# Kernel optimization log

Hardware: AMD Instinct MI355X
Metric: run time of the kernel (lower is better)

## Reference

```python
import jax, jax.numpy as jnp
import numpy as np

NUM_INPUTS = 784
NUM_OUTPUTS = 784
WIDTH_POW = 10
WIDTH = 2 ** WIDTH_POW          # 1024
HALF = WIDTH // 2               # 512
DEPTH = 8
BDEPTH = 10
DEGREE = 2
BATCH = 4096

# knots from the source: tensor([-256..256]) / 32
_KNOTS = np.array([-256., -128., -64., -32., -16., -8., -4., -2., -1., 0.,
                   1., 2., 4., 8., 16., 32., 64., 128., 256.], dtype=np.float32) / 32.0
# clamped (open) knot vector: repeat endpoints `degree` times
_T = np.concatenate([np.full(DEGREE, _KNOTS[0]), _KNOTS, np.full(DEGREE, _KNOTS[-1])]).astype(np.float32)
SPLINE_DIM = len(_T) - DEGREE - 1  # 20 basis functions


def _bspline_basis(x):
    """Cox-de Boor B-spline basis, vectorized over all elements of x.
    Returns basis of shape x.shape + (SPLINE_DIM,)."""
    t = jnp.asarray(_T)
    x = jnp.clip(x, _T[0], _T[-1] - 1e-6)  # clamp to knot span (eval domain)
    xe = x[..., None]
    B = ((xe >= t[:-1]) & (xe < t[1:])).astype(x.dtype)  # degree-0 indicators
    for k in range(1, DEGREE + 1):
        tj, tjk = t[:-(k + 1)], t[k:-1]
        tj1, tjk1 = t[1:-k], t[k + 1:]
        d1, d2 = tjk - tj, tjk1 - tj1
        w1 = jnp.where(d1 > 0, (xe - tj) / jnp.where(d1 > 0, d1, 1.0), 0.0)
        w2 = jnp.where(d2 > 0, (tjk1 - xe) / jnp.where(d2 > 0, d2, 1.0), 0.0)
        B = w1 * B[..., :-1] + w2 * B[..., 1:]
    return B  # [..., SPLINE_DIM]


def _butterfly(X, params):
    """OrthogonalButterfly.forward. params: [HALF, BDEPTH]. X: [B, WIDTH]."""
    Bsz = X.shape[0]
    for d in range(BDEPTH):
        theta = params[:, d]
        c, s = jnp.cos(theta), jnp.sin(theta)
        X0, X1 = X[:, :HALF], X[:, HALF:]
        n0 = X0 * c + X1 * s
        n1 = -X0 * s + X1 * c
        # perm[i] = i//2 (even) / i//2 + half (odd) == interleave halves
        X = jnp.stack([n0, n1], axis=2).reshape(Bsz, WIDTH)
    return X


def _forward(X, butterfly_params, spline_coefs):
    Bsz = X.shape[0]
    X = jnp.concatenate([X, jnp.zeros((Bsz, WIDTH - NUM_INPUTS), X.dtype)], axis=1)
    for i in range(DEPTH):
        X = _butterfly(X, butterfly_params[i])
        if i != DEPTH - 1:
            # ReversibleActivation: X0 += spline(X1), per-column spline coefs
            X0, X1 = X[:, :HALF], X[:, HALF:]
            act = jnp.einsum('bwd,wd->bw', _bspline_basis(X1), spline_coefs[i])
            X = jnp.concatenate([X0 + act, X1], axis=1)
    return X[:, :NUM_OUTPUTS]


def setup_inputs() -> dict:
    key = jax.random.key(0)
    k1, k2, k3 = jax.random.split(key, 3)
    X = jax.random.normal(k1, (BATCH, NUM_INPUTS), dtype=jnp.float32)
    butterfly_params = jax.random.uniform(k2, (DEPTH, HALF, BDEPTH), dtype=jnp.float32) * (2.0 * np.pi)
    spline_coefs = jax.random.uniform(k3, (DEPTH - 1, HALF, SPLINE_DIM), dtype=jnp.float32) * 0.2 - 0.1
    return {"X": X, "butterfly_params": butterfly_params, "spline_coefs": spline_coefs}


def reference(X, butterfly_params, spline_coefs):
    return _forward(X, butterfly_params, spline_coefs)
```

## Files before the change

### kernel.cpp

```cpp
#include <hip/hip_runtime.h>

#define NIN 784
#define WIDTH 1024
#define HALF 512
#define DEPTH 8
#define BDEPTH 10
#define BATCH 4096
#define SPLINE_DIM 20
#define NQ 18

__device__ float d_T[23] = {
  -8.f, -8.f, -8.f, -4.f, -2.f, -1.f, -0.5f, -0.25f, -0.125f, -0.0625f,
  -0.03125f, 0.f, 0.03125f, 0.0625f, 0.125f, 0.25f, 0.5f, 1.f, 2.f, 4.f,
  8.f, 8.f, 8.f };

__global__ void prep_kernel(const float* __restrict__ bp,
                            const float* __restrict__ sc,
                            float2* __restrict__ cs,
                            float4* __restrict__ qt) {
  int gid = blockIdx.x * 256 + threadIdx.x;
  if (gid < DEPTH * BDEPTH * 1024) {
    int slot = gid & 1023;
    int d = (gid >> 10) % BDEPTH;
    int i = gid / (BDEPTH * 1024);
    int n = 0;
#pragma unroll
    for (int b = 0; b < 10; ++b) {
      int src = b - d; if (src < 0) src += 10;
      n |= ((slot >> src) & 1) << b;
    }
    int pj = n & 511;
    float theta = bp[(i * HALF + pj) * BDEPTH + d];
    float c = cosf(theta), s = sinf(theta);
    cs[gid] = make_float2(c, (n & 512) ? -s : s);
  }
  int gid2 = gid - DEPTH * BDEPTH * 1024;
  if (gid2 >= 0 && gid2 < (DEPTH - 1) * NQ * HALF) {
    int w = gid2 & 511;
    int mi = (gid2 >> 9) % NQ;
    int i = gid2 / (NQ * HALF);
    int m = mi + 2;
    const float* cf = sc + (i * HALF + w) * SPLINE_DIM;
    double c0 = cf[mi], c1 = cf[mi + 1], c2 = cf[mi + 2];
    double tm1 = d_T[m - 1], tm = d_T[m], tp1 = d_T[m + 1], tp2 = d_T[m + 2];
    double h = tp1 - tm;
    double us[3] = { 0.0, 0.5 * h, 0.75 * h };
    double y[3];
#pragma unroll
    for (int k = 0; k < 3; ++k) {
      double x = tm + us[k];
      double left1 = x - tm, right1 = tp1 - x, left2 = x - tm1, right2 = tp2 - x;
      double inv1 = 1.0 / (tp1 - tm);
      double N0 = right1 * inv1, N1 = left1 * inv1;
      double temp0 = N0 / (tp1 - tm1);
      double B0 = right1 * temp0;
      double saved = left2 * temp0;
      double temp1 = N1 / (tp2 - tm);
      double B1 = right2 * temp1 + saved;
      double B2 = left1 * temp1;
      y[k] = c0 * B0 + c1 * B1 + c2 * B2;
    }
    double d1 = y[1] - y[0], d2 = y[2] - y[0];
    double u1 = us[1], u2 = us[2];
    double det = u1 * u2 * (u2 - u1);
    double Bq = (d1 * u2 * u2 - d2 * u1 * u1) / det;
    double Cq = (d2 * u1 - d1 * u2) / det;
    qt[gid2] = make_float4((float)y[0], (float)Bq, (float)Cq, (float)tm);
  }
}

template <int M>
__device__ __forceinline__ float shfx(float x) {
  if constexpr (M == 1)
    return __int_as_float(__builtin_amdgcn_mov_dpp(__float_as_int(x), 0xB1, 0xF, 0xF, true));
  else if constexpr (M == 2)
    return __int_as_float(__builtin_amdgcn_mov_dpp(__float_as_int(x), 0x4E, 0xF, 0xF, true));
  else if constexpr (M == 4)
    return __int_as_float(__builtin_amdgcn_ds_swizzle(__float_as_int(x), 0x101F));
  else if constexpr (M == 8)
    return __int_as_float(__builtin_amdgcn_ds_swizzle(__float_as_int(x), 0x201F));
  else if constexpr (M == 16)
    return __int_as_float(__builtin_amdgcn_ds_swizzle(__float_as_int(x), 0x401F));
  else
    return __shfl_xor(x, 32, 64);
}

__device__ __forceinline__ float qspline(float x, const float4* __restrict__ qL, int w) {
  x = fminf(fmaxf(x, -8.0f), 7.9999990f);
  float ax = fabsf(x);
  unsigned bits = __float_as_uint(ax);
  int e = (int)(bits >> 23) - 127;
  int ce = e + ((bits & 0x7fffffu) ? 1 : 0);
  int m = (x > 0.f) ? (17 + e) : (5 - ce);
  m = (ax < 0.03125f) ? ((x < 0.f) ? 10 : 11) : m;
  float4 qc = qL[(m - 2) * HALF + w];
  float u = x - qc.w;
  return fmaf(u, fmaf(u, qc.z, qc.y), qc.x);
}

typedef __attribute__((address_space(3))) unsigned int lds_u32;
typedef __attribute__((address_space(1))) const unsigned int glb_u32;

__device__ __forceinline__ void stage_async(const float2* __restrict__ src,
                                            float2* dst, int wv) {
#pragma unroll
  for (int k = 0; k < 5; ++k) {
    int seg = k * 8 + wv;
    const char* g = (const char*)src + seg * 1024 + (threadIdx.x & 63) * 16;
    char* l = (char*)dst + seg * 1024;
    __builtin_amdgcn_global_load_lds((glb_u32*)g, (lds_u32*)l, 16, 0, 0);
  }
}

#define CSTEPL(P, sl, dd) do {                                                \
    const int _mr = 8 >> (dd);                                                \
    _Pragma("unroll") for (int r = 0; r < 16; ++r)                            \
      if ((r & _mr) == 0) {                                                   \
        float2 v = P[(sl) * 1024 + r * 64 + lane];                            \
        float a0 = s0[r], b0 = s0[r + _mr];                                   \
        s0[r]       = fmaf(a0, v.x, b0 * v.y);                                \
        s0[r + _mr] = fmaf(b0, v.x, -(a0 * v.y));                             \
        float a1 = s1[r], b1 = s1[r + _mr];                                   \
        s1[r]       = fmaf(a1, v.x, b1 * v.y);                                \
        s1[r + _mr] = fmaf(b1, v.x, -(a1 * v.y));                             \
      }                                                                       \
  } while (0)

#define LSTEPL(P, sl, MM) do {                                                \
    _Pragma("unroll") for (int r = 0; r < 16; ++r) {                          \
      float2 v = P[(sl) * 1024 + r * 64 + lane];                              \
      float p0 = shfx<MM>(s0[r]);                                             \
      float p1 = shfx<MM>(s1[r]);                                             \
      s0[r] = fmaf(s0[r], v.x, p0 * v.y);                                     \
      s1[r] = fmaf(s1[r], v.x, p1 * v.y);                                     \
    }                                                                         \
  } while (0)

__global__ __launch_bounds__(512, 1) void fwd_kernel(
    const float* __restrict__ X, const float2* __restrict__ cs,
    const float4* __restrict__ qt, float* __restrict__ out) {
  __shared__ float2 csA[5 * 1024];
  __shared__ float2 csB[5 * 1024];
  int tid = threadIdx.x;
  int lane = tid & 63;
  int wv = tid >> 6;
  int row0 = blockIdx.x * 16 + wv * 2;

  const float* x0p = X + (long)row0 * NIN;
  const float* x1p = X + (long)(row0 + 1) * NIN;
  float s0[16], s1[16];
#pragma unroll
  for (int r = 0; r < 16; ++r) {
    int w = r * 64 + lane;
    bool in = (w < NIN);
    s0[r] = in ? x0p[w] : 0.f;
    s1[r] = in ? x1p[w] : 0.f;
  }

  stage_async(cs, csA, wv);

#pragma unroll 1
  for (int i = 0; i < DEPTH; ++i) {
    const float2* csL = cs + i * (BDEPTH * 1024);

    __syncthreads();
    stage_async(csL + 5 * 1024, csB, wv);
    asm volatile("s_waitcnt vmcnt(5)" ::: "memory");
    __syncthreads();
    CSTEPL(csA, 0, 0);
    CSTEPL(csA, 1, 1);
    CSTEPL(csA, 2, 2);
    CSTEPL(csA, 3, 3);
    LSTEPL(csA, 4, 32);

    __syncthreads();
    stage_async(cs + ((i + 1) & 7) * (BDEPTH * 1024), csA, wv);
    asm volatile("s_waitcnt vmcnt(5)" ::: "memory");
    __syncthreads();
    LSTEPL(csB, 0, 16);
    LSTEPL(csB, 1, 8);
    LSTEPL(csB, 2, 4);
    LSTEPL(csB, 3, 2);
    LSTEPL(csB, 4, 1);

    if (i != DEPTH - 1) {
      const float4* qL = qt + i * (NQ * HALF);
#pragma unroll
      for (int r = 8; r < 16; ++r) {
        int w = ((r - 8) << 6) | lane;
        s0[r - 8] += qspline(s0[r], qL, w);
        s1[r - 8] += qspline(s1[r], qL, w);
      }
    }
  }

  float* o0 = out + (long)row0 * NIN;
  float* o1 = out + (long)(row0 + 1) * NIN;
#pragma unroll
  for (int r = 0; r < 13; ++r) {
    int w = r * 64 + lane;
    if (w < NIN) { o0[w] = s0[r]; o1[w] = s1[r]; }
  }
}

extern "C" void kernel_launch(void* const* d_in, const int* in_sizes, int n_in,
                              void* d_out, int out_size, void* d_ws, size_t ws_size,
                              hipStream_t stream) {
  const float* X  = (const float*)d_in[0];
  const float* bp = (const float*)d_in[1];
  const float* sc = (const float*)d_in[2];
  float* out = (float*)d_out;

  float2* cs = (float2*)d_ws;
  float4* qt = (float4*)((char*)d_ws + DEPTH * BDEPTH * 1024 * sizeof(float2));

  int prep_threads = DEPTH * BDEPTH * 1024 + (DEPTH - 1) * NQ * HALF;
  prep_kernel<<<(prep_threads + 255) / 256, 256, 0, stream>>>(bp, sc, cs, qt);
  fwd_kernel<<<BATCH / 16, 512, 0, stream>>>(X, cs, qt, out);
}
```

Measured before the change: 70.86 us.

## Stage full layer coefficients per buffer, pair lane steps, pack rows as float2

Changes the coefficient staging so each double-buffered LDS buffer holds a whole layer's 10 butterfly stages. This halves the number of barriers per layer. The prep kernel now writes the six lane-shuffle stages as interleaved pairs so one float4 LDS read serves two stages. The two batch rows are packed into float2 vectors so the compiler can emit packed FMA instructions. LDS use doubles to 160KB, which stays within one block per CU but reduces staging-overlap slack.

New measurement: 66.35 us. 6.4% less time.

```diff
diff --git a/kernel.cpp b/kernel.cpp
--- a/kernel.cpp
+++ b/kernel.cpp
@@ -8,6 +8,8 @@
 #define BATCH 4096
 #define SPLINE_DIM 20
 #define NQ 18
+
+typedef __attribute__((ext_vector_type(2))) float f32x2;
 
 __device__ float d_T[23] = {
   -8.f, -8.f, -8.f, -4.f, -2.f, -1.f, -0.5f, -0.25f, -0.125f, -0.0625f,
@@ -32,7 +34,14 @@
     int pj = n & 511;
     float theta = bp[(i * HALF + pj) * BDEPTH + d];
     float c = cosf(theta), s = sinf(theta);
-    cs[gid] = make_float2(c, (n & 512) ? -s : s);
+    float2 val = make_float2(c, (n & 512) ? -s : s);
+    int off;
+    if (d < 4) off = i * 10240 + d * 1024 + slot;
+    else {
+      int p = (d - 4) >> 1, sub = (d - 4) & 1;
+      off = i * 10240 + 4096 + p * 2048 + slot * 2 + sub;
+    }
+    cs[off] = val;
   }
   int gid2 = gid - DEPTH * BDEPTH * 1024;
   if (gid2 >= 0 && gid2 < (DEPTH - 1) * NQ * HALF) {
@@ -104,7 +113,7 @@
 __device__ __forceinline__ void stage_async(const float2* __restrict__ src,
                                             float2* dst, int wv) {
 #pragma unroll
-  for (int k = 0; k < 5; ++k) {
+  for (int k = 0; k < 10; ++k) {
     int seg = k * 8 + wv;
     const char* g = (const char*)src + seg * 1024 + (threadIdx.x & 63) * 16;
     char* l = (char*)dst + seg * 1024;
@@ -112,35 +121,36 @@
   }
 }
 
-#define CSTEPL(P, sl, dd) do {                                                \
+#define CSTEPL(dd) do {                                                       \
     const int _mr = 8 >> (dd);                                                \
     _Pragma("unroll") for (int r = 0; r < 16; ++r)                            \
       if ((r & _mr) == 0) {                                                   \
-        float2 v = P[(sl) * 1024 + r * 64 + lane];                            \
-        float a0 = s0[r], b0 = s0[r + _mr];                                   \
-        s0[r]       = fmaf(a0, v.x, b0 * v.y);                                \
-        s0[r + _mr] = fmaf(b0, v.x, -(a0 * v.y));                             \
-        float a1 = s1[r], b1 = s1[r + _mr];                                   \
-        s1[r]       = fmaf(a1, v.x, b1 * v.y);                                \
-        s1[r + _mr] = fmaf(b1, v.x, -(a1 * v.y));                             \
+        float2 v = cur[(dd) * 1024 + r * 64 + lane];                          \
+        f32x2 a = st[r], b2 = st[r + _mr];                                    \
+        f32x2 vc = {v.x, v.x}, vs = {v.y, v.y};                               \
+        st[r]       = __builtin_elementwise_fma(a, vc, b2 * vs);              \
+        st[r + _mr] = __builtin_elementwise_fma(b2, vc, -(a * vs));           \
       }                                                                       \
   } while (0)
 
-#define LSTEPL(P, sl, MM) do {                                                \
+#define LPAIR(p, M1, M2) do {                                                 \
+    const float4* _pp = (const float4*)(cur + 4096 + (p) * 2048);             \
     _Pragma("unroll") for (int r = 0; r < 16; ++r) {                          \
-      float2 v = P[(sl) * 1024 + r * 64 + lane];                              \
-      float p0 = shfx<MM>(s0[r]);                                             \
-      float p1 = shfx<MM>(s1[r]);                                             \
-      s0[r] = fmaf(s0[r], v.x, p0 * v.y);                                     \
-      s1[r] = fmaf(s1[r], v.x, p1 * v.y);                                     \
+      float4 v = _pp[r * 64 + lane];                                          \
+      f32x2 q1 = { shfx<M1>(st[r].x), shfx<M1>(st[r].y) };                    \
+      st[r] = __builtin_elementwise_fma(st[r], (f32x2){v.x, v.x},             \
+                                        q1 * (f32x2){v.y, v.y});              \
+      f32x2 q2 = { shfx<M2>(st[r].x), shfx<M2>(st[r].y) };                    \
+      st[r] = __builtin_elementwise_fma(st[r], (f32x2){v.z, v.z},             \
+                                        q2 * (f32x2){v.w, v.w});              \
     }                                                                         \
   } while (0)
 
 __global__ __launch_bounds__(512, 1) void fwd_kernel(
     const float* __restrict__ X, const float2* __restrict__ cs,
     const float4* __restrict__ qt, float* __restrict__ out) {
-  __shared__ float2 csA[5 * 1024];
-  __shared__ float2 csB[5 * 1024];
+  __shared__ float2 bufA[10240];
+  __shared__ float2 bufB[10240];
   int tid = threadIdx.x;
   int lane = tid & 63;
   int wv = tid >> 6;
@@ -148,48 +158,41 @@
 
   const float* x0p = X + (long)row0 * NIN;
   const float* x1p = X + (long)(row0 + 1) * NIN;
-  float s0[16], s1[16];
+  f32x2 st[16];
 #pragma unroll
   for (int r = 0; r < 16; ++r) {
     int w = r * 64 + lane;
     bool in = (w < NIN);
-    s0[r] = in ? x0p[w] : 0.f;
-    s1[r] = in ? x1p[w] : 0.f;
-  }
-
-  stage_async(cs, csA, wv);
+    st[r] = (f32x2){ in ? x0p[w] : 0.f, in ? x1p[w] : 0.f };
+  }
+
+  stage_async(cs, bufA, wv);
 
 #pragma unroll 1
   for (int i = 0; i < DEPTH; ++i) {
-    const float2* csL = cs + i * (BDEPTH * 1024);
+    const float2* cur = (i & 1) ? bufB : bufA;
+    float2* nxt = (i & 1) ? bufA : bufB;
 
     __syncthreads();
-    stage_async(csL + 5 * 1024, csB, wv);
-    asm volatile("s_waitcnt vmcnt(5)" ::: "memory");
+    stage_async(cs + ((i + 1) & 7) * 10240, nxt, wv);
+    asm volatile("s_waitcnt vmcnt(10)" ::: "memory");
     __syncthreads();
-    CSTEPL(csA, 0, 0);
-    CSTEPL(csA, 1, 1);
-    CSTEPL(csA, 2, 2);
-    CSTEPL(csA, 3, 3);
-    LSTEPL(csA, 4, 32);
-
-    __syncthreads();
-    stage_async(cs + ((i + 1) & 7) * (BDEPTH * 1024), csA, wv);
-    asm volatile("s_waitcnt vmcnt(5)" ::: "memory");
-    __syncthreads();
-    LSTEPL(csB, 0, 16);
-    LSTEPL(csB, 1, 8);
-    LSTEPL(csB, 2, 4);
-    LSTEPL(csB, 3, 2);
-    LSTEPL(csB, 4, 1);
+
+    CSTEPL(0);
+    CSTEPL(1);
+    CSTEPL(2);
+    CSTEPL(3);
+    LPAIR(0, 32, 16);
+    LPAIR(1, 8, 4);
+    LPAIR(2, 2, 1);
 
     if (i != DEPTH - 1) {
       const float4* qL = qt + i * (NQ * HALF);
 #pragma unroll
       for (int r = 8; r < 16; ++r) {
         int w = ((r - 8) << 6) | lane;
-        s0[r - 8] += qspline(s0[r], qL, w);
-        s1[r - 8] += qspline(s1[r], qL, w);
+        st[r - 8].x += qspline(st[r].x, qL, w);
+        st[r - 8].y += qspline(st[r].y, qL, w);
       }
     }
   }
@@ -199,7 +202,7 @@
 #pragma unroll
   for (int r = 0; r < 13; ++r) {
     int w = r * 64 + lane;
-    if (w < NIN) { o0[w] = s0[r]; o1[w] = s1[r]; }
+    if (w < NIN) { o0[w] = st[r].x; o1[w] = st[r].y; }
   }
 }
 
```
